# Kernel optimization log

Hardware: AMD Instinct MI355X
Metric: run time of the kernel (lower is better)

The kernel has to match this reference:

```python
import jax, jax.numpy as jnp
import numpy as np

B, S = 128, 200
Q, K, V, C, SUM = 20000, 128, 128, 64, 128


def setup_inputs() -> dict:
    key = jax.random.key(0)
    ks = jax.random.split(key, 14)
    stdev = 1.0 / np.sqrt(C + K)  # NTM-style memory init bound

    def lin_w(k, fan_in, shape):
        b = 1.0 / np.sqrt(fan_in)
        return jax.random.uniform(k, shape, jnp.float32, -b, b)

    # embeddings with padding_idx=0 zeroed (PAD_INDEX=0)
    q_emb = jax.random.normal(ks[0], (Q + 1, K), jnp.float32).at[0].set(0.0)
    i_emb = jax.random.normal(ks[1], (2 * Q + 1, V), jnp.float32).at[0].set(0.0)
    key_memory = jax.random.uniform(ks[2], (K, C), jnp.float32, -stdev, stdev)
    init_value_memory = jax.random.uniform(ks[3], (V, C), jnp.float32, -stdev, stdev)
    erase_W = lin_w(ks[4], V, (V, V))
    erase_b = lin_w(ks[5], V, (V,))
    add_W = lin_w(ks[6], V, (V, V))
    add_b = lin_w(ks[7], V, (V,))
    summ_W = lin_w(ks[8], V + K, (V + K, SUM))
    summ_b = lin_w(ks[9], V + K, (SUM,))
    out_W = lin_w(ks[10], SUM, (SUM, 1))
    out_b = lin_w(ks[11], SUM, (1,))
    inp = jax.random.randint(ks[12], (B, S), 0, 2 * Q + 1)
    target_id = jax.random.randint(ks[13], (B,), 0, Q + 1)
    return dict(q_emb=q_emb, i_emb=i_emb, key_memory=key_memory,
                init_value_memory=init_value_memory,
                erase_W=erase_W, erase_b=erase_b, add_W=add_W, add_b=add_b,
                summ_W=summ_W, summ_b=summ_b, out_W=out_W, out_b=out_b,
                input=inp, target_id=target_id)


def reference(q_emb, i_emb, key_memory, init_value_memory,
              erase_W, erase_b, add_W, add_b,
              summ_W, summ_b, out_W, out_b,
              input, target_id):
    Qn = q_emb.shape[0] - 1
    bsz = input.shape[0]
    # map interaction index -> question id
    qid = input - Qn * (input > Qn).astype(input.dtype)          # (B,S)
    # all per-step quantities are independent of memory state -> precompute
    iv = i_emb[input]                                            # (B,S,V)
    e = jax.nn.sigmoid(iv @ erase_W + erase_b)                   # (B,S,V)
    a = jnp.tanh(iv @ add_W + add_b)                             # (B,S,V)
    w = jax.nn.softmax(q_emb[qid] @ key_memory, axis=-1)         # (B,S,C)

    mem0 = jnp.broadcast_to(init_value_memory, (bsz,) + init_value_memory.shape)  # (B,V,C)

    def step(mem, xs):
        e_t, a_t, w_t = xs                                       # (B,V),(B,V),(B,C)
        erase = e_t[:, :, None] * w_t[:, None, :]                # rank-1 outer, (B,V,C)
        add = a_t[:, :, None] * w_t[:, None, :]
        mem = mem * (1.0 - erase) + add
        return mem, None

    xs = (jnp.swapaxes(e, 0, 1), jnp.swapaxes(a, 0, 1), jnp.swapaxes(w, 0, 1))
    mem, _ = jax.lax.scan(step, mem0, xs)                        # (B,V,C)

    qv = q_emb[target_id]                                        # (B,K)
    wt = jax.nn.softmax(qv @ key_memory, axis=-1)                # (B,C)
    read = jnp.einsum('bvc,bc->bv', mem, wt)                     # (B,V)
    summ = jnp.tanh(jnp.concatenate([read, qv], axis=-1) @ summ_W + summ_b)
    return summ @ out_W + out_b                                  # (B,1), pre-sigmoid
```

## Files before the change

kernel.cpp:

```cpp
#include <hip/hip_runtime.h>
#include <hip/hip_bf16.h>

#define B_ 128
#define S_ 200
#define QN_ 20000
#define V_ 128
#define K_ 128
#define C_ 64
#define SUM_ 128

using short8 = __attribute__((ext_vector_type(8))) short;
using f32x4  = __attribute__((ext_vector_type(4))) float;

template<bool BF>
__device__ __forceinline__ float ld(const void* p, long long i) {
    if (BF) return __bfloat162float(((const __hip_bfloat16*)p)[i]);
    return ((const float*)p)[i];
}
template<bool BF>
__device__ __forceinline__ float2 ld2(const void* p, long long i) {
    if (BF) {
        __hip_bfloat162 v = ((const __hip_bfloat162*)p)[i];
        return make_float2(__bfloat162float(v.x), __bfloat162float(v.y));
    }
    return ((const float2*)p)[i];
}

__device__ __forceinline__ unsigned short f2bf(float v) {
    __hip_bfloat16 h = __float2bfloat16(v);
    unsigned short u;
    __builtin_memcpy(&u, &h, 2);
    return u;
}

__device__ __forceinline__ int probe_flag_wave(const void* erase_b) {
    const unsigned* w = (const unsigned*)erase_b;
    const int lane = threadIdx.x & 63;
    const unsigned lo = w[lane] & 0xffffu;
    const float f = __uint_as_float(lo << 16);
    const unsigned long long bal = __ballot(!(fabsf(f) <= 0.5f));
    return (__popcll(bal) <= 8) ? 1 : 0;
}

__global__ __launch_bounds__(256) void dkvmn_prepack(
    const void* erase_W, const void* add_W, const void* key_memory,
    const void* erase_b, unsigned short* __restrict__ wpack)
{
    const int bf = probe_flag_wave(erase_b);
    const int fid = blockIdx.x * 256 + threadIdx.x;
    if (fid >= 5120) return;
    const int lane = fid & 63;
    const int ks = (fid >> 6) & 3;
    const int wv = (fid >> 8) & 3;
    const int q  = fid >> 10;
    const int nt = wv + 4 * q;
    const void* Wsrc;
    int ncol, ldn;
    if (q < 2)      { Wsrc = erase_W;    ncol = nt * 16 + (lane & 15);        ldn = 128; }
    else if (q < 4) { Wsrc = add_W;      ncol = (nt - 8) * 16 + (lane & 15);  ldn = 128; }
    else            { Wsrc = key_memory; ncol = (nt - 16) * 16 + (lane & 15); ldn = 64; }
    const int k8 = (lane >> 4) * 8;
    unsigned short o[8];
    #pragma unroll
    for (int jj = 0; jj < 8; ++jj) {
        const long long idx = (long long)(ks * 32 + k8 + jj) * ldn + ncol;
        const float v = bf ? ld<true>(Wsrc, idx) : ld<false>(Wsrc, idx);
        o[jj] = f2bf(v);
    }
    *(uint4*)(wpack + (size_t)fid * 8) = *(const uint4*)o;
}

template<bool BF>
__device__ __forceinline__ void phase1_mfma_body(
    const void* q_emb, const void* i_emb,
    const void* erase_b, const void* add_b,
    const int* __restrict__ input, const unsigned short* __restrict__ wpack,
    float* __restrict__ e_buf, float* __restrict__ a_buf, float* __restrict__ w_buf,
    unsigned short* ivA, unsigned short* qvA, float* wlog, int* sidx, int* sqid)
{
    const int p0 = blockIdx.x * 64;
    const int t = threadIdx.x;
    const int wv = t >> 6;
    const int lane = t & 63;
    const int lrow = lane & 15;
    const int lk8 = (lane >> 4) * 8;

    if (t < 64) {
        const int ix = input[p0 + t];
        sidx[t] = ix;
        sqid[t] = ix > QN_ ? ix - QN_ : ix;
    }
    __syncthreads();

    #pragma unroll
    for (int r = 0; r < 8; ++r) {
        const int j = t + 256 * r;
        const int tensor = j >> 10;
        const int row = (j >> 4) & 63;
        const int seg = j & 15;
        const int gr = tensor ? sqid[row] : sidx[row];
        unsigned short* dst = (tensor ? qvA : ivA) + row * 136 + seg * 8;
        if (BF) {
            const unsigned short* src = (const unsigned short*)(tensor ? q_emb : i_emb);
            *(uint4*)dst = *(const uint4*)(src + (long long)gr * 128 + seg * 8);
        } else {
            const float* src = (const float*)(tensor ? q_emb : i_emb) + (long long)gr * 128 + seg * 8;
            const float4 f0 = *(const float4*)src;
            const float4 f1 = *(const float4*)(src + 4);
            unsigned short o[8] = {f2bf(f0.x), f2bf(f0.y), f2bf(f0.z), f2bf(f0.w),
                                   f2bf(f1.x), f2bf(f1.y), f2bf(f1.z), f2bf(f1.w)};
            *(uint4*)dst = *(const uint4*)o;
        }
    }

    short8 bfr[5][4];
    int nco[5];
    float biasq[4];
    #pragma unroll
    for (int q = 0; q < 5; ++q) {
        const int nt = wv + 4 * q;
        if (q < 2)      nco[q] = nt * 16 + lrow;
        else if (q < 4) nco[q] = (nt - 8) * 16 + lrow;
        else            nco[q] = (nt - 16) * 16 + lrow;
        if (q < 2)      biasq[q] = ld<BF>(erase_b, nco[q]);
        else if (q < 4) biasq[q] = ld<BF>(add_b, nco[q]);
        #pragma unroll
        for (int ks = 0; ks < 4; ++ks)
            bfr[q][ks] = *(const short8*)(wpack +
                ((size_t)(((q * 4 + wv) * 4 + ks) * 64 + lane)) * 8);
    }
    __syncthreads();

    for (int mt = 0; mt < 4; ++mt) {
        short8 afr[4];
        const unsigned short* ar = ivA + (mt * 16 + lrow) * 136 + lk8;
        #pragma unroll
        for (int ks = 0; ks < 4; ++ks)
            afr[ks] = *(const short8*)(ar + ks * 32);
        #pragma unroll
        for (int q = 0; q < 4; ++q) {
            f32x4 acc = {0.f, 0.f, 0.f, 0.f};
            #pragma unroll
            for (int ks = 0; ks < 4; ++ks)
                acc = __builtin_amdgcn_mfma_f32_16x16x32_bf16(afr[ks], bfr[q][ks], acc, 0, 0, 0);
            float* dst = (q < 2) ? e_buf : a_buf;
            const int ncol = nco[q];
            const float bb = biasq[q];
            #pragma unroll
            for (int r = 0; r < 4; ++r) {
                const int prow = p0 + mt * 16 + (lane >> 4) * 4 + r;
                const float y = acc[r] + bb;
                dst[(size_t)prow * V_ + ncol] =
                    (q < 2) ? 1.f / (1.f + expf(-y)) : tanhf(y);
            }
        }
    }
    for (int mt = 0; mt < 4; ++mt) {
        short8 afr[4];
        const unsigned short* ar = qvA + (mt * 16 + lrow) * 136 + lk8;
        #pragma unroll
        for (int ks = 0; ks < 4; ++ks)
            afr[ks] = *(const short8*)(ar + ks * 32);
        f32x4 acc = {0.f, 0.f, 0.f, 0.f};
        #pragma unroll
        for (int ks = 0; ks < 4; ++ks)
            acc = __builtin_amdgcn_mfma_f32_16x16x32_bf16(afr[ks], bfr[4][ks], acc, 0, 0, 0);
        #pragma unroll
        for (int r = 0; r < 4; ++r)
            wlog[(mt * 16 + (lane >> 4) * 4 + r) * 68 + nco[4]] = acc[r];
    }
    __syncthreads();

    {
        const int row = t >> 2;
        const int cs = t & 3;
        const float* wr = &wlog[row * 68 + cs * 16];
        float v[16];
        #pragma unroll
        for (int ii = 0; ii < 4; ++ii)
            *(float4*)&v[ii * 4] = *(const float4*)&wr[ii * 4];
        float m = v[0];
        #pragma unroll
        for (int ii = 1; ii < 16; ++ii) m = fmaxf(m, v[ii]);
        m = fmaxf(m, __shfl_xor(m, 1, 64));
        m = fmaxf(m, __shfl_xor(m, 2, 64));
        float s = 0.f;
        #pragma unroll
        for (int ii = 0; ii < 16; ++ii) { v[ii] = expf(v[ii] - m); s += v[ii]; }
        s += __shfl_xor(s, 1, 64);
        s += __shfl_xor(s, 2, 64);
        const float inv = 1.f / s;
        float* wout = w_buf + (size_t)(p0 + row) * C_ + cs * 16;
        #pragma unroll
        for (int ii = 0; ii < 4; ++ii)
            *(float4*)&wout[ii * 4] = make_float4(v[ii*4] * inv, v[ii*4+1] * inv,
                                                  v[ii*4+2] * inv, v[ii*4+3] * inv);
    }
}

__global__ __launch_bounds__(256) void dkvmn_phase1_mfma(
    const void* q_emb, const void* i_emb,
    const void* erase_b, const void* add_b,
    const int* __restrict__ input, const unsigned short* __restrict__ wpack,
    float* e_buf, float* a_buf, float* w_buf)
{
    __shared__ unsigned short ivA[64 * 136];
    __shared__ unsigned short qvA[64 * 136];
    __shared__ float wlog[64 * 68];
    __shared__ int sidx[64], sqid[64];
    if (probe_flag_wave(erase_b))
        phase1_mfma_body<true>(q_emb, i_emb, erase_b, add_b, input, wpack,
                               e_buf, a_buf, w_buf, ivA, qvA, wlog, sidx, sqid);
    else
        phase1_mfma_body<false>(q_emb, i_emb, erase_b, add_b, input, wpack,
                                e_buf, a_buf, w_buf, ivA, qvA, wlog, sidx, sqid);
}

__device__ __forceinline__ void scan_step44(float mem[4][4], float4 e4, float4 a4,
                                            float4 w4) {
    const float ev[4] = {e4.x, e4.y, e4.z, e4.w};
    const float av[4] = {a4.x, a4.y, a4.z, a4.w};
    const float wvv[4] = {w4.x, w4.y, w4.z, w4.w};
    #pragma unroll
    for (int i = 0; i < 4; ++i)
        #pragma unroll
        for (int j = 0; j < 4; ++j)
            mem[i][j] = fmaf(wvv[j], fmaf(-mem[i][j], ev[i], av[i]), mem[i][j]);
}

template<bool BF>
__device__ __forceinline__ void phase2_body(
    const void* q_emb, const void* key_memory, const void* init_value_memory,
    const int* __restrict__ target_id,
    const float* __restrict__ e_buf, const float* __restrict__ a_buf,
    const float* __restrict__ w_buf, float* __restrict__ part_buf,
    float* wtl)
{
    const int bid = blockIdx.x;
    const int b = bid & 127;
    const int ch = bid >> 7;
    const int t = threadIdx.x;
    const int vg = t >> 3;
    const int cg = t & 7;
    const int v0 = vg * 4;
    const int c0 = ch * 32 + cg * 4;

    float mem[4][4];
    #pragma unroll
    for (int i = 0; i < 4; ++i) {
        const float2 m01 = ld2<BF>(init_value_memory, ((v0 + i) * C_ + c0) >> 1);
        const float2 m23 = ld2<BF>(init_value_memory, ((v0 + i) * C_ + c0 + 2) >> 1);
        mem[i][0] = m01.x; mem[i][1] = m01.y; mem[i][2] = m23.x; mem[i][3] = m23.y;
    }

    const float* eb = e_buf + (size_t)b * S_ * V_ + v0;
    const float* ab = a_buf + (size_t)b * S_ * V_ + v0;
    const float* wb = w_buf + (size_t)b * S_ * C_ + c0;

    float4 pe[5], pa[5], pw[5];
    #pragma unroll
    for (int k = 0; k < 5; ++k) {
        pe[k] = *(const float4*)(eb + (size_t)k * V_);
        pa[k] = *(const float4*)(ab + (size_t)k * V_);
        pw[k] = *(const float4*)(wb + (size_t)k * C_);
    }
    for (int s0 = 0; s0 < 195; s0 += 5) {
        #pragma unroll
        for (int k = 0; k < 5; ++k) {
            const float4 E = pe[k], A = pa[k], W = pw[k];
            const size_t sn = (size_t)(s0 + k + 5);
            pe[k] = *(const float4*)(eb + sn * V_);
            pa[k] = *(const float4*)(ab + sn * V_);
            pw[k] = *(const float4*)(wb + sn * C_);
            scan_step44(mem, E, A, W);
        }
    }
    #pragma unroll
    for (int k = 0; k < 5; ++k)
        scan_step44(mem, pe[k], pa[k], pw[k]);

    if (t < 64) {
        const long long qrow = (long long)target_id[b] * K_;
        float logit = 0.f;
        #pragma unroll 8
        for (int i = 0; i < K_; ++i)
            logit += ld<BF>(q_emb, qrow + i) * ld<BF>(key_memory, i * C_ + t);
        float m = logit;
        for (int off = 32; off > 0; off >>= 1)
            m = fmaxf(m, __shfl_xor(m, off, 64));
        const float ex = expf(logit - m);
        float ssum = ex;
        for (int off = 32; off > 0; off >>= 1)
            ssum += __shfl_xor(ssum, off, 64);
        wtl[t] = ex / ssum;
    }
    __syncthreads();

    float wt4[4];
    *(float4*)wt4 = *(const float4*)&wtl[c0];
    float red[4];
    #pragma unroll
    for (int i = 0; i < 4; ++i)
        red[i] = mem[i][0]*wt4[0] + mem[i][1]*wt4[1] + mem[i][2]*wt4[2] + mem[i][3]*wt4[3];
    #pragma unroll
    for (int off = 1; off < 8; off <<= 1) {
        #pragma unroll
        for (int i = 0; i < 4; ++i)
            red[i] += __shfl_xor(red[i], off, 64);
    }
    if (cg == 0)
        *(float4*)(part_buf + ((size_t)ch * B_ + b) * V_ + v0) =
            make_float4(red[0], red[1], red[2], red[3]);
}

__global__ __launch_bounds__(256) void dkvmn_phase2(
    const void* q_emb, const void* key_memory, const void* init_value_memory,
    const void* erase_b,
    const int* __restrict__ target_id,
    const float* e_buf, const float* a_buf, const float* w_buf,
    float* part_buf)
{
    __shared__ float wtl[C_];
    if (probe_flag_wave(erase_b))
        phase2_body<true>(q_emb, key_memory, init_value_memory, target_id,
                          e_buf, a_buf, w_buf, part_buf, wtl);
    else
        phase2_body<false>(q_emb, key_memory, init_value_memory, target_id,
                           e_buf, a_buf, w_buf, part_buf, wtl);
}

template<bool BF>
__device__ __forceinline__ void phase3_body(
    const void* q_emb, const void* summ_W, const void* summ_b,
    const void* out_W, const void* out_b,
    const int* __restrict__ target_id, const float* __restrict__ part_buf,
    void* outp, float* summl)
{
    const int b = blockIdx.x;
    const int t = threadIdx.x;
    const long long qrow = (long long)target_id[b] * K_;
    const float* pb0 = part_buf + (size_t)b * V_;
    const float* pb1 = part_buf + (size_t)(B_ + b) * V_;

    float acc = ld<BF>(summ_b, t);
    #pragma unroll 8
    for (int i = 0; i < 128; ++i)
        acc += (pb0[i] + pb1[i]) * ld<BF>(summ_W, i * SUM_ + t);
    #pragma unroll 8
    for (int i = 0; i < 128; ++i)
        acc += ld<BF>(q_emb, qrow + i) * ld<BF>(summ_W, (128 + i) * SUM_ + t);
    summl[t] = tanhf(acc);
    __syncthreads();

    if (t < 64) {
        float pacc = summl[t] * ld<BF>(out_W, t) + summl[t + 64] * ld<BF>(out_W, t + 64);
        for (int off = 32; off > 0; off >>= 1)
            pacc += __shfl_xor(pacc, off, 64);
        if (t == 0) {
            const float res = pacc + ld<BF>(out_b, 0);
            if (BF) ((__hip_bfloat16*)outp)[b] = __float2bfloat16(res);
            else    ((float*)outp)[b] = res;
        }
    }
}

__global__ __launch_bounds__(128) void dkvmn_phase3(
    const void* q_emb, const void* summ_W, const void* summ_b,
    const void* out_W, const void* out_b, const void* erase_b,
    const int* __restrict__ target_id, const float* part_buf,
    void* outp)
{
    __shared__ float summl[SUM_];
    if (probe_flag_wave(erase_b))
        phase3_body<true>(q_emb, summ_W, summ_b, out_W, out_b, target_id,
                          part_buf, outp, summl);
    else
        phase3_body<false>(q_emb, summ_W, summ_b, out_W, out_b, target_id,
                           part_buf, outp, summl);
}

extern "C" void kernel_launch(void* const* d_in, const int* in_sizes, int n_in,
                              void* d_out, int out_size, void* d_ws, size_t ws_size,
                              hipStream_t stream) {
    const void* q_emb             = d_in[0];
    const void* i_emb             = d_in[1];
    const void* key_memory        = d_in[2];
    const void* init_value_memory = d_in[3];
    const void* erase_W           = d_in[4];
    const void* erase_b           = d_in[5];
    const void* add_W             = d_in[6];
    const void* add_b             = d_in[7];
    const void* summ_W            = d_in[8];
    const void* summ_b            = d_in[9];
    const void* out_W             = d_in[10];
    const void* out_b             = d_in[11];
    const int* input     = (const int*)d_in[12];
    const int* target_id = (const int*)d_in[13];

    float* e_buf    = (float*)d_ws;
    float* a_buf    = e_buf + (size_t)B_ * S_ * V_;
    float* w_buf    = a_buf + (size_t)B_ * S_ * V_;
    float* part_buf = w_buf + (size_t)B_ * S_ * C_;
    unsigned short* wpack = (unsigned short*)(part_buf + (size_t)2 * B_ * V_);

    dkvmn_prepack<<<20, 256, 0, stream>>>(erase_W, add_W, key_memory, erase_b, wpack);
    dkvmn_phase1_mfma<<<(B_ * S_) / 64, 256, 0, stream>>>(
        q_emb, i_emb, erase_b, add_b, input, wpack, e_buf, a_buf, w_buf);
    dkvmn_phase2<<<2 * B_, 256, 0, stream>>>(
        q_emb, key_memory, init_value_memory, erase_b, target_id,
        e_buf, a_buf, w_buf, part_buf);
    dkvmn_phase3<<<B_, 128, 0, stream>>>(
        q_emb, summ_W, summ_b, out_W, out_b, erase_b, target_id, part_buf, d_out);
}
```

Measured before the change: 149.9 us.

## Split scan over value halves and shrink phase1 tiles; use fast exp math

The recurrent scan kernel now splits each batch element's value dimension into two halves, so it launches 4*B blocks instead of 2*B. Each thread now carries a 2x4 memory tile instead of 4x4, which shortens the serial per-thread work and spreads it over more CUs. The embedding/MFMA projection kernel processes 32 rows per block instead of 64, doubling the block count and halving shared memory per block. Sigmoid, tanh and the softmax exps switch to __expf-based fast approximations, which trades a little precision for fewer instructions.

After: 165.0 us. 10.1% more time.

```diff
diff --git a/kernel.cpp b/kernel.cpp
--- a/kernel.cpp
+++ b/kernel.cpp
@@ -11,6 +11,9 @@
 
 using short8 = __attribute__((ext_vector_type(8))) short;
 using f32x4  = __attribute__((ext_vector_type(4))) float;
+
+__device__ __forceinline__ float fast_sigmoid(float x) { return 1.f / (1.f + __expf(-x)); }
+__device__ __forceinline__ float fast_tanh(float x)    { return 1.f - 2.f / (__expf(2.f * x) + 1.f); }
 
 template<bool BF>
 __device__ __forceinline__ float ld(const void* p, long long i) {
@@ -78,14 +81,14 @@
     float* __restrict__ e_buf, float* __restrict__ a_buf, float* __restrict__ w_buf,
     unsigned short* ivA, unsigned short* qvA, float* wlog, int* sidx, int* sqid)
 {
-    const int p0 = blockIdx.x * 64;
+    const int p0 = blockIdx.x * 32;
     const int t = threadIdx.x;
     const int wv = t >> 6;
     const int lane = t & 63;
     const int lrow = lane & 15;
     const int lk8 = (lane >> 4) * 8;
 
-    if (t < 64) {
+    if (t < 32) {
         const int ix = input[p0 + t];
         sidx[t] = ix;
         sqid[t] = ix > QN_ ? ix - QN_ : ix;
@@ -93,10 +96,10 @@
     __syncthreads();
 
     #pragma unroll
-    for (int r = 0; r < 8; ++r) {
+    for (int r = 0; r < 4; ++r) {
         const int j = t + 256 * r;
-        const int tensor = j >> 10;
-        const int row = (j >> 4) & 63;
+        const int tensor = j >> 9;
+        const int row = (j >> 4) & 31;
         const int seg = j & 15;
         const int gr = tensor ? sqid[row] : sidx[row];
         unsigned short* dst = (tensor ? qvA : ivA) + row * 136 + seg * 8;
@@ -131,7 +134,8 @@
     }
     __syncthreads();
 
-    for (int mt = 0; mt < 4; ++mt) {
+    #pragma unroll
+    for (int mt = 0; mt < 2; ++mt) {
         short8 afr[4];
         const unsigned short* ar = ivA + (mt * 16 + lrow) * 136 + lk8;
         #pragma unroll
@@ -151,11 +155,12 @@
                 const int prow = p0 + mt * 16 + (lane >> 4) * 4 + r;
                 const float y = acc[r] + bb;
                 dst[(size_t)prow * V_ + ncol] =
-                    (q < 2) ? 1.f / (1.f + expf(-y)) : tanhf(y);
+                    (q < 2) ? fast_sigmoid(y) : fast_tanh(y);
             }
         }
     }
-    for (int mt = 0; mt < 4; ++mt) {
+    #pragma unroll
+    for (int mt = 0; mt < 2; ++mt) {
         short8 afr[4];
         const unsigned short* ar = qvA + (mt * 16 + lrow) * 136 + lk8;
         #pragma unroll
@@ -172,29 +177,28 @@
     __syncthreads();
 
     {
-        const int row = t >> 2;
-        const int cs = t & 3;
-        const float* wr = &wlog[row * 68 + cs * 16];
-        float v[16];
-        #pragma unroll
-        for (int ii = 0; ii < 4; ++ii)
-            *(float4*)&v[ii * 4] = *(const float4*)&wr[ii * 4];
+        const int row = t >> 3;
+        const int cs = t & 7;
+        const float* wr = &wlog[row * 68 + cs * 8];
+        float v[8];
+        *(float4*)&v[0] = *(const float4*)&wr[0];
+        *(float4*)&v[4] = *(const float4*)&wr[4];
         float m = v[0];
         #pragma unroll
-        for (int ii = 1; ii < 16; ++ii) m = fmaxf(m, v[ii]);
+        for (int ii = 1; ii < 8; ++ii) m = fmaxf(m, v[ii]);
         m = fmaxf(m, __shfl_xor(m, 1, 64));
         m = fmaxf(m, __shfl_xor(m, 2, 64));
+        m = fmaxf(m, __shfl_xor(m, 4, 64));
         float s = 0.f;
         #pragma unroll
-        for (int ii = 0; ii < 16; ++ii) { v[ii] = expf(v[ii] - m); s += v[ii]; }
+        for (int ii = 0; ii < 8; ++ii) { v[ii] = __expf(v[ii] - m); s += v[ii]; }
         s += __shfl_xor(s, 1, 64);
         s += __shfl_xor(s, 2, 64);
+        s += __shfl_xor(s, 4, 64);
         const float inv = 1.f / s;
-        float* wout = w_buf + (size_t)(p0 + row) * C_ + cs * 16;
-        #pragma unroll
-        for (int ii = 0; ii < 4; ++ii)
-            *(float4*)&wout[ii * 4] = make_float4(v[ii*4] * inv, v[ii*4+1] * inv,
-                                                  v[ii*4+2] * inv, v[ii*4+3] * inv);
+        float* wout = w_buf + (size_t)(p0 + row) * C_ + cs * 8;
+        *(float4*)&wout[0] = make_float4(v[0]*inv, v[1]*inv, v[2]*inv, v[3]*inv);
+        *(float4*)&wout[4] = make_float4(v[4]*inv, v[5]*inv, v[6]*inv, v[7]*inv);
     }
 }
 
@@ -204,10 +208,10 @@
     const int* __restrict__ input, const unsigned short* __restrict__ wpack,
     float* e_buf, float* a_buf, float* w_buf)
 {
-    __shared__ unsigned short ivA[64 * 136];
-    __shared__ unsigned short qvA[64 * 136];
-    __shared__ float wlog[64 * 68];
-    __shared__ int sidx[64], sqid[64];
+    __shared__ unsigned short ivA[32 * 136];
+    __shared__ unsigned short qvA[32 * 136];
+    __shared__ float wlog[32 * 68];
+    __shared__ int sidx[32], sqid[32];
     if (probe_flag_wave(erase_b))
         phase1_mfma_body<true>(q_emb, i_emb, erase_b, add_b, input, wpack,
                                e_buf, a_buf, w_buf, ivA, qvA, wlog, sidx, sqid);
@@ -216,13 +220,13 @@
                                 e_buf, a_buf, w_buf, ivA, qvA, wlog, sidx, sqid);
 }
 
-__device__ __forceinline__ void scan_step44(float mem[4][4], float4 e4, float4 a4,
+__device__ __forceinline__ void scan_step24(float mem[2][4], float2 e2, float2 a2,
                                             float4 w4) {
-    const float ev[4] = {e4.x, e4.y, e4.z, e4.w};
-    const float av[4] = {a4.x, a4.y, a4.z, a4.w};
+    const float ev[2] = {e2.x, e2.y};
+    const float av[2] = {a2.x, a2.y};
     const float wvv[4] = {w4.x, w4.y, w4.z, w4.w};
     #pragma unroll
-    for (int i = 0; i < 4; ++i)
+    for (int i = 0; i < 2; ++i)
         #pragma unroll
         for (int j = 0; j < 4; ++j)
             mem[i][j] = fmaf(wvv[j], fmaf(-mem[i][j], ev[i], av[i]), mem[i][j]);
@@ -238,16 +242,18 @@
 {
     const int bid = blockIdx.x;
     const int b = bid & 127;
-    const int ch = bid >> 7;
+    const int sub = bid >> 7;
+    const int ch = sub & 1;
+    const int vh = sub >> 1;
     const int t = threadIdx.x;
     const int vg = t >> 3;
     const int cg = t & 7;
-    const int v0 = vg * 4;
+    const int v0 = vh * 64 + vg * 2;
     const int c0 = ch * 32 + cg * 4;
 
-    float mem[4][4];
-    #pragma unroll
-    for (int i = 0; i < 4; ++i) {
+    float mem[2][4];
+    #pragma unroll
+    for (int i = 0; i < 2; ++i) {
         const float2 m01 = ld2<BF>(init_value_memory, ((v0 + i) * C_ + c0) >> 1);
         const float2 m23 = ld2<BF>(init_value_memory, ((v0 + i) * C_ + c0 + 2) >> 1);
         mem[i][0] = m01.x; mem[i][1] = m01.y; mem[i][2] = m23.x; mem[i][3] = m23.y;
@@ -257,27 +263,29 @@
     const float* ab = a_buf + (size_t)b * S_ * V_ + v0;
     const float* wb = w_buf + (size_t)b * S_ * C_ + c0;
 
-    float4 pe[5], pa[5], pw[5];
+    float2 pe[5], pa[5];
+    float4 pw[5];
     #pragma unroll
     for (int k = 0; k < 5; ++k) {
-        pe[k] = *(const float4*)(eb + (size_t)k * V_);
-        pa[k] = *(const float4*)(ab + (size_t)k * V_);
+        pe[k] = *(const float2*)(eb + (size_t)k * V_);
+        pa[k] = *(const float2*)(ab + (size_t)k * V_);
         pw[k] = *(const float4*)(wb + (size_t)k * C_);
     }
     for (int s0 = 0; s0 < 195; s0 += 5) {
         #pragma unroll
         for (int k = 0; k < 5; ++k) {
-            const float4 E = pe[k], A = pa[k], W = pw[k];
+            const float2 E = pe[k], A = pa[k];
+            const float4 W = pw[k];
             const size_t sn = (size_t)(s0 + k + 5);
-            pe[k] = *(const float4*)(eb + sn * V_);
-            pa[k] = *(const float4*)(ab + sn * V_);
+            pe[k] = *(const float2*)(eb + sn * V_);
+            pa[k] = *(const float2*)(ab + sn * V_);
             pw[k] = *(const float4*)(wb + sn * C_);
-            scan_step44(mem, E, A, W);
+            scan_step24(mem, E, A, W);
         }
     }
     #pragma unroll
     for (int k = 0; k < 5; ++k)
-        scan_step44(mem, pe[k], pa[k], pw[k]);
+        scan_step24(mem, pe[k], pa[k], pw[k]);
 
     if (t < 64) {
         const long long qrow = (long long)target_id[b] * K_;
@@ -288,7 +296,7 @@
         float m = logit;
         for (int off = 32; off > 0; off >>= 1)
             m = fmaxf(m, __shfl_xor(m, off, 64));
-        const float ex = expf(logit - m);
+        const float ex = __expf(logit - m);
         float ssum = ex;
         for (int off = 32; off > 0; off >>= 1)
             ssum += __shfl_xor(ssum, off, 64);
@@ -298,19 +306,19 @@
 
     float wt4[4];
     *(float4*)wt4 = *(const float4*)&wtl[c0];
-    float red[4];
-    #pragma unroll
-    for (int i = 0; i < 4; ++i)
+    float red[2];
+    #pragma unroll
+    for (int i = 0; i < 2; ++i)
         red[i] = mem[i][0]*wt4[0] + mem[i][1]*wt4[1] + mem[i][2]*wt4[2] + mem[i][3]*wt4[3];
     #pragma unroll
     for (int off = 1; off < 8; off <<= 1) {
         #pragma unroll
-        for (int i = 0; i < 4; ++i)
+        for (int i = 0; i < 2; ++i)
             red[i] += __shfl_xor(red[i], off, 64);
     }
     if (cg == 0)
-        *(float4*)(part_buf + ((size_t)ch * B_ + b) * V_ + v0) =
-            make_float4(red[0], red[1], red[2], red[3]);
+        *(float2*)(part_buf + ((size_t)ch * B_ + b) * V_ + v0) =
+            make_float2(red[0], red[1]);
 }
 
 __global__ __launch_bounds__(256) void dkvmn_phase2(
@@ -349,7 +357,7 @@
     #pragma unroll 8
     for (int i = 0; i < 128; ++i)
         acc += ld<BF>(q_emb, qrow + i) * ld<BF>(summ_W, (128 + i) * SUM_ + t);
-    summl[t] = tanhf(acc);
+    summl[t] = fast_tanh(acc);
     __syncthreads();
 
     if (t < 64) {
@@ -404,9 +412,9 @@
     unsigned short* wpack = (unsigned short*)(part_buf + (size_t)2 * B_ * V_);
 
     dkvmn_prepack<<<20, 256, 0, stream>>>(erase_W, add_W, key_memory, erase_b, wpack);
-    dkvmn_phase1_mfma<<<(B_ * S_) / 64, 256, 0, stream>>>(
+    dkvmn_phase1_mfma<<<(B_ * S_) / 32, 256, 0, stream>>>(
         q_emb, i_emb, erase_b, add_b, input, wpack, e_buf, a_buf, w_buf);
-    dkvmn_phase2<<<2 * B_, 256, 0, stream>>>(
+    dkvmn_phase2<<<4 * B_, 256, 0, stream>>>(
         q_emb, key_memory, init_value_memory, erase_b, target_id,
         e_buf, a_buf, w_buf, part_buf);
     dkvmn_phase3<<<B_, 128, 0, stream>>>(
```

## Parallelize recurrence over time chunks with affine-composition scan and fused combine

Applied to the files above, without the earlier changes.

Splits the 200-step memory recurrence into 8 chunks of 25 steps. Each chunk computes its composed affine map (product of decays and accumulated offset) per memory cell, so 1024 blocks run instead of 256 blocks doing sequential 200-step loops. A new combine kernel applies the chunk maps to the initial memory, performs the read and the summary/output MLP, and replaces the old phase2/phase3 pair. Chunk maps are stored as fp16 pairs, which cuts traffic but risks precision loss: the products of decays can underflow and the offsets lose precision. The change also switches sigmoid, tanh and exp to fast __expf variants.

Measured after the change: 154.6 us. +3.1%, slower.

```diff
diff --git a/kernel.cpp b/kernel.cpp
--- a/kernel.cpp
+++ b/kernel.cpp
@@ -1,5 +1,6 @@
 #include <hip/hip_runtime.h>
 #include <hip/hip_bf16.h>
+#include <hip/hip_fp16.h>
 
 #define B_ 128
 #define S_ 200
@@ -8,9 +9,14 @@
 #define K_ 128
 #define C_ 64
 #define SUM_ 128
+#define NCH 8
+#define CL 25
 
 using short8 = __attribute__((ext_vector_type(8))) short;
 using f32x4  = __attribute__((ext_vector_type(4))) float;
+
+__device__ __forceinline__ float fast_sigmoid(float x) { return 1.f / (1.f + __expf(-x)); }
+__device__ __forceinline__ float fast_tanh(float x)    { return 1.f - 2.f / (__expf(2.f * x) + 1.f); }
 
 template<bool BF>
 __device__ __forceinline__ float ld(const void* p, long long i) {
@@ -151,7 +157,7 @@
                 const int prow = p0 + mt * 16 + (lane >> 4) * 4 + r;
                 const float y = acc[r] + bb;
                 dst[(size_t)prow * V_ + ncol] =
-                    (q < 2) ? 1.f / (1.f + expf(-y)) : tanhf(y);
+                    (q < 2) ? fast_sigmoid(y) : fast_tanh(y);
             }
         }
     }
@@ -186,7 +192,7 @@
         m = fmaxf(m, __shfl_xor(m, 2, 64));
         float s = 0.f;
         #pragma unroll
-        for (int ii = 0; ii < 16; ++ii) { v[ii] = expf(v[ii] - m); s += v[ii]; }
+        for (int ii = 0; ii < 16; ++ii) { v[ii] = __expf(v[ii] - m); s += v[ii]; }
         s += __shfl_xor(s, 1, 64);
         s += __shfl_xor(s, 2, 64);
         const float inv = 1.f / s;
@@ -216,71 +222,101 @@
                                 e_buf, a_buf, w_buf, ivA, qvA, wlog, sidx, sqid);
 }
 
-__device__ __forceinline__ void scan_step44(float mem[4][4], float4 e4, float4 a4,
-                                            float4 w4) {
-    const float ev[4] = {e4.x, e4.y, e4.z, e4.w};
-    const float av[4] = {a4.x, a4.y, a4.z, a4.w};
-    const float wvv[4] = {w4.x, w4.y, w4.z, w4.w};
-    #pragma unroll
-    for (int i = 0; i < 4; ++i)
-        #pragma unroll
-        for (int j = 0; j < 4; ++j)
-            mem[i][j] = fmaf(wvv[j], fmaf(-mem[i][j], ev[i], av[i]), mem[i][j]);
-}
-
-template<bool BF>
-__device__ __forceinline__ void phase2_body(
-    const void* q_emb, const void* key_memory, const void* init_value_memory,
-    const int* __restrict__ target_id,
+__global__ __launch_bounds__(256) void dkvmn_scan(
     const float* __restrict__ e_buf, const float* __restrict__ a_buf,
-    const float* __restrict__ w_buf, float* __restrict__ part_buf,
-    float* wtl)
+    const float* __restrict__ w_buf, __half2* __restrict__ du)
 {
     const int bid = blockIdx.x;
     const int b = bid & 127;
-    const int ch = bid >> 7;
+    const int chunk = bid >> 7;
     const int t = threadIdx.x;
     const int vg = t >> 3;
     const int cg = t & 7;
-    const int v0 = vg * 4;
-    const int c0 = ch * 32 + cg * 4;
-
-    float mem[4][4];
+    const int v0 = vg * 4, c0 = cg * 8;
+
+    float ym[4][8], Dm[4][8];
+    #pragma unroll
+    for (int i = 0; i < 4; ++i)
+        #pragma unroll
+        for (int j = 0; j < 8; ++j) { ym[i][j] = 0.f; Dm[i][j] = 1.f; }
+
+    const float* eb = e_buf + ((size_t)b * S_ + chunk * CL) * V_ + v0;
+    const float* ab = a_buf + ((size_t)b * S_ + chunk * CL) * V_ + v0;
+    const float* wb = w_buf + ((size_t)b * S_ + chunk * CL) * C_ + c0;
+
+    #define SSTEP(E, A, W0, W1)                                                \
+        do {                                                                   \
+            const float ev[4] = {(E).x, (E).y, (E).z, (E).w};                  \
+            const float av[4] = {(A).x, (A).y, (A).z, (A).w};                  \
+            const float wvv[8] = {(W0).x, (W0).y, (W0).z, (W0).w,              \
+                                  (W1).x, (W1).y, (W1).z, (W1).w};             \
+            _Pragma("unroll")                                                  \
+            for (int i = 0; i < 4; ++i) {                                      \
+                _Pragma("unroll")                                              \
+                for (int j = 0; j < 8; ++j) {                                  \
+                    const float d = fmaf(-ev[i], wvv[j], 1.f);                 \
+                    Dm[i][j] *= d;                                             \
+                    ym[i][j] = fmaf(d, ym[i][j], av[i] * wvv[j]);              \
+                }                                                              \
+            }                                                                  \
+        } while (0)
+
+    float4 pe[2], pa[2], pw0[2], pw1[2];
+    #pragma unroll
+    for (int k = 0; k < 2; ++k) {
+        pe[k]  = *(const float4*)(eb + (size_t)k * V_);
+        pa[k]  = *(const float4*)(ab + (size_t)k * V_);
+        pw0[k] = *(const float4*)(wb + (size_t)k * C_);
+        pw1[k] = *(const float4*)(wb + (size_t)k * C_ + 4);
+    }
+    for (int s0 = 0; s0 < 22; s0 += 2) {
+        #pragma unroll
+        for (int k = 0; k < 2; ++k) {
+            const float4 E = pe[k], A = pa[k], W0 = pw0[k], W1 = pw1[k];
+            const size_t sn = (size_t)(s0 + k + 2);
+            pe[k]  = *(const float4*)(eb + sn * V_);
+            pa[k]  = *(const float4*)(ab + sn * V_);
+            pw0[k] = *(const float4*)(wb + sn * C_);
+            pw1[k] = *(const float4*)(wb + sn * C_ + 4);
+            SSTEP(E, A, W0, W1);
+        }
+    }
+    {
+        const float4 te  = *(const float4*)(eb + (size_t)24 * V_);
+        const float4 ta  = *(const float4*)(ab + (size_t)24 * V_);
+        const float4 tw0 = *(const float4*)(wb + (size_t)24 * C_);
+        const float4 tw1 = *(const float4*)(wb + (size_t)24 * C_ + 4);
+        SSTEP(pe[0], pa[0], pw0[0], pw1[0]);
+        SSTEP(pe[1], pa[1], pw0[1], pw1[1]);
+        SSTEP(te, ta, tw0, tw1);
+    }
+    #undef SSTEP
+
+    __half2* dbase = du + ((size_t)(chunk * B_ + b) * (V_ * C_));
     #pragma unroll
     for (int i = 0; i < 4; ++i) {
-        const float2 m01 = ld2<BF>(init_value_memory, ((v0 + i) * C_ + c0) >> 1);
-        const float2 m23 = ld2<BF>(init_value_memory, ((v0 + i) * C_ + c0 + 2) >> 1);
-        mem[i][0] = m01.x; mem[i][1] = m01.y; mem[i][2] = m23.x; mem[i][3] = m23.y;
-    }
-
-    const float* eb = e_buf + (size_t)b * S_ * V_ + v0;
-    const float* ab = a_buf + (size_t)b * S_ * V_ + v0;
-    const float* wb = w_buf + (size_t)b * S_ * C_ + c0;
-
-    float4 pe[5], pa[5], pw[5];
-    #pragma unroll
-    for (int k = 0; k < 5; ++k) {
-        pe[k] = *(const float4*)(eb + (size_t)k * V_);
-        pa[k] = *(const float4*)(ab + (size_t)k * V_);
-        pw[k] = *(const float4*)(wb + (size_t)k * C_);
-    }
-    for (int s0 = 0; s0 < 195; s0 += 5) {
-        #pragma unroll
-        for (int k = 0; k < 5; ++k) {
-            const float4 E = pe[k], A = pa[k], W = pw[k];
-            const size_t sn = (size_t)(s0 + k + 5);
-            pe[k] = *(const float4*)(eb + sn * V_);
-            pa[k] = *(const float4*)(ab + sn * V_);
-            pw[k] = *(const float4*)(wb + sn * C_);
-            scan_step44(mem, E, A, W);
-        }
-    }
-    #pragma unroll
-    for (int k = 0; k < 5; ++k)
-        scan_step44(mem, pe[k], pa[k], pw[k]);
+        __half2 h[8];
+        #pragma unroll
+        for (int j = 0; j < 8; ++j)
+            h[j] = __floats2half2_rn(Dm[i][j], ym[i][j]);
+        __half2* dst = dbase + (v0 + i) * C_ + c0;
+        *(uint4*)dst = *(const uint4*)&h[0];
+        *(uint4*)(dst + 4) = *(const uint4*)&h[4];
+    }
+}
+
+template<bool BF>
+__device__ __forceinline__ void combine_body(
+    const void* q_emb, const void* key_memory, const void* init_value_memory,
+    const void* summ_W, const void* summ_b, const void* out_W, const void* out_b,
+    const int* __restrict__ target_id, const __half2* __restrict__ du,
+    void* outp, float* wtl, float* readl, float* summl)
+{
+    const int b = blockIdx.x;
+    const int t = threadIdx.x;
+    const long long qrow = (long long)target_id[b] * K_;
 
     if (t < 64) {
-        const long long qrow = (long long)target_id[b] * K_;
         float logit = 0.f;
         #pragma unroll 8
         for (int i = 0; i < K_; ++i)
@@ -288,95 +324,74 @@
         float m = logit;
         for (int off = 32; off > 0; off >>= 1)
             m = fmaxf(m, __shfl_xor(m, off, 64));
-        const float ex = expf(logit - m);
+        const float ex = __expf(logit - m);
         float ssum = ex;
         for (int off = 32; off > 0; off >>= 1)
             ssum += __shfl_xor(ssum, off, 64);
         wtl[t] = ex / ssum;
     }
-    __syncthreads();
-
-    float wt4[4];
-    *(float4*)wt4 = *(const float4*)&wtl[c0];
-    float red[4];
-    #pragma unroll
-    for (int i = 0; i < 4; ++i)
-        red[i] = mem[i][0]*wt4[0] + mem[i][1]*wt4[1] + mem[i][2]*wt4[2] + mem[i][3]*wt4[3];
-    #pragma unroll
-    for (int off = 1; off < 8; off <<= 1) {
-        #pragma unroll
-        for (int i = 0; i < 4; ++i)
-            red[i] += __shfl_xor(red[i], off, 64);
-    }
-    if (cg == 0)
-        *(float4*)(part_buf + ((size_t)ch * B_ + b) * V_ + v0) =
-            make_float4(red[0], red[1], red[2], red[3]);
-}
-
-__global__ __launch_bounds__(256) void dkvmn_phase2(
-    const void* q_emb, const void* key_memory, const void* init_value_memory,
-    const void* erase_b,
-    const int* __restrict__ target_id,
-    const float* e_buf, const float* a_buf, const float* w_buf,
-    float* part_buf)
-{
-    __shared__ float wtl[C_];
-    if (probe_flag_wave(erase_b))
-        phase2_body<true>(q_emb, key_memory, init_value_memory, target_id,
-                          e_buf, a_buf, w_buf, part_buf, wtl);
-    else
-        phase2_body<false>(q_emb, key_memory, init_value_memory, target_id,
-                           e_buf, a_buf, w_buf, part_buf, wtl);
-}
-
-template<bool BF>
-__device__ __forceinline__ void phase3_body(
-    const void* q_emb, const void* summ_W, const void* summ_b,
-    const void* out_W, const void* out_b,
-    const int* __restrict__ target_id, const float* __restrict__ part_buf,
-    void* outp, float* summl)
-{
-    const int b = blockIdx.x;
-    const int t = threadIdx.x;
-    const long long qrow = (long long)target_id[b] * K_;
-    const float* pb0 = part_buf + (size_t)b * V_;
-    const float* pb1 = part_buf + (size_t)(B_ + b) * V_;
-
-    float acc = ld<BF>(summ_b, t);
+
+    const int v = t >> 1;
+    const int c0 = (t & 1) * 32;
+    float mem[32];
     #pragma unroll 8
-    for (int i = 0; i < 128; ++i)
-        acc += (pb0[i] + pb1[i]) * ld<BF>(summ_W, i * SUM_ + t);
-    #pragma unroll 8
-    for (int i = 0; i < 128; ++i)
-        acc += ld<BF>(q_emb, qrow + i) * ld<BF>(summ_W, (128 + i) * SUM_ + t);
-    summl[t] = tanhf(acc);
-    __syncthreads();
-
+    for (int k = 0; k < 32; ++k)
+        mem[k] = ld<BF>(init_value_memory, v * C_ + c0 + k);
+    #pragma unroll
+    for (int ch = 0; ch < NCH; ++ch) {
+        const __half2* dsrc = du + ((size_t)(ch * B_ + b) * (V_ * C_)) + v * C_ + c0;
+        #pragma unroll
+        for (int k = 0; k < 32; ++k) {
+            const float2 f = __half22float2(dsrc[k]);
+            mem[k] = fmaf(f.x, mem[k], f.y);
+        }
+    }
+    __syncthreads();
+
+    float pacc = 0.f;
+    #pragma unroll
+    for (int k = 0; k < 32; ++k)
+        pacc += mem[k] * wtl[c0 + k];
+    pacc += __shfl_xor(pacc, 1, 64);
+    if ((t & 1) == 0) readl[v] = pacc;
+    __syncthreads();
+
+    if (t < 128) {
+        float acc = ld<BF>(summ_b, t);
+        #pragma unroll 8
+        for (int i = 0; i < 128; ++i)
+            acc += readl[i] * ld<BF>(summ_W, i * SUM_ + t);
+        #pragma unroll 8
+        for (int i = 0; i < 128; ++i)
+            acc += ld<BF>(q_emb, qrow + i) * ld<BF>(summ_W, (128 + i) * SUM_ + t);
+        summl[t] = fast_tanh(acc);
+    }
+    __syncthreads();
     if (t < 64) {
-        float pacc = summl[t] * ld<BF>(out_W, t) + summl[t + 64] * ld<BF>(out_W, t + 64);
+        float oacc = summl[t] * ld<BF>(out_W, t) + summl[t + 64] * ld<BF>(out_W, t + 64);
         for (int off = 32; off > 0; off >>= 1)
-            pacc += __shfl_xor(pacc, off, 64);
+            oacc += __shfl_xor(oacc, off, 64);
         if (t == 0) {
-            const float res = pacc + ld<BF>(out_b, 0);
+            const float res = oacc + ld<BF>(out_b, 0);
             if (BF) ((__hip_bfloat16*)outp)[b] = __float2bfloat16(res);
             else    ((float*)outp)[b] = res;
         }
     }
 }
 
-__global__ __launch_bounds__(128) void dkvmn_phase3(
-    const void* q_emb, const void* summ_W, const void* summ_b,
-    const void* out_W, const void* out_b, const void* erase_b,
-    const int* __restrict__ target_id, const float* part_buf,
-    void* outp)
-{
-    __shared__ float summl[SUM_];
+__global__ __launch_bounds__(256) void dkvmn_combine(
+    const void* q_emb, const void* key_memory, const void* init_value_memory,
+    const void* summ_W, const void* summ_b, const void* out_W, const void* out_b,
+    const void* erase_b, const int* __restrict__ target_id,
+    const __half2* __restrict__ du, void* outp)
+{
+    __shared__ float wtl[C_], readl[V_], summl[SUM_];
     if (probe_flag_wave(erase_b))
-        phase3_body<true>(q_emb, summ_W, summ_b, out_W, out_b, target_id,
-                          part_buf, outp, summl);
+        combine_body<true>(q_emb, key_memory, init_value_memory, summ_W, summ_b,
+                           out_W, out_b, target_id, du, outp, wtl, readl, summl);
     else
-        phase3_body<false>(q_emb, summ_W, summ_b, out_W, out_b, target_id,
-                           part_buf, outp, summl);
+        combine_body<false>(q_emb, key_memory, init_value_memory, summ_W, summ_b,
+                            out_W, out_b, target_id, du, outp, wtl, readl, summl);
 }
 
 extern "C" void kernel_launch(void* const* d_in, const int* in_sizes, int n_in,
@@ -397,18 +412,17 @@
     const int* input     = (const int*)d_in[12];
     const int* target_id = (const int*)d_in[13];
 
-    float* e_buf    = (float*)d_ws;
-    float* a_buf    = e_buf + (size_t)B_ * S_ * V_;
-    float* w_buf    = a_buf + (size_t)B_ * S_ * V_;
-    float* part_buf = w_buf + (size_t)B_ * S_ * C_;
-    unsigned short* wpack = (unsigned short*)(part_buf + (size_t)2 * B_ * V_);
+    float* e_buf = (float*)d_ws;
+    float* a_buf = e_buf + (size_t)B_ * S_ * V_;
+    float* w_buf = a_buf + (size_t)B_ * S_ * V_;
+    unsigned short* wpack = (unsigned short*)(w_buf + (size_t)B_ * S_ * C_);
+    __half2* du = (__half2*)(wpack + 5120 * 8);
 
     dkvmn_prepack<<<20, 256, 0, stream>>>(erase_W, add_W, key_memory, erase_b, wpack);
     dkvmn_phase1_mfma<<<(B_ * S_) / 64, 256, 0, stream>>>(
         q_emb, i_emb, erase_b, add_b, input, wpack, e_buf, a_buf, w_buf);
-    dkvmn_phase2<<<2 * B_, 256, 0, stream>>>(
-        q_emb, key_memory, init_value_memory, erase_b, target_id,
-        e_buf, a_buf, w_buf, part_buf);
-    dkvmn_phase3<<<B_, 128, 0, stream>>>(
-        q_emb, summ_W, summ_b, out_W, out_b, erase_b, target_id, part_buf, d_out);
-}
+    dkvmn_scan<<<NCH * B_, 256, 0, stream>>>(e_buf, a_buf, w_buf, du);
+    dkvmn_combine<<<B_, 256, 0, stream>>>(
+        q_emb, key_memory, init_value_memory, summ_W, summ_b, out_W, out_b,
+        erase_b, target_id, du, d_out);
+}
```
